# Optimization experiments

Measured on AMD Instinct MI355X. Metric: run time of the kernel, lower is better.

## Reference

```python
import jax, jax.numpy as jnp
import numpy as np
from functools import partial

K = 8  # seq_len from constructor


def _normalizer_impl(p, K):
    # 3-step Newton-Raphson solve for alpha s.t. sum_i (1 - exp(alpha*log(1-p_i))) == K
    N = p.shape[-1]
    y = jnp.log(1.0 - p)                        # (*, N)
    alpha = jnp.full(p.shape[:-1], float(K), dtype=p.dtype)
    for _ in range(3):
        e = jnp.exp(alpha[..., None] * y)       # (*, N)
        err = e.sum(axis=-1) + (K - N)          # (*,)
        d = (e * y).sum(axis=-1)                # (*,)
        alpha = alpha - err / d
    # analytic derivative used by the custom torch backward (ctx.deriv)
    deriv = alpha[..., None] * e / (d[..., None] * (1.0 - p))
    return alpha, deriv


@partial(jax.custom_vjp, nondiff_argnums=(1,))
def compute_normalizer(p, K):
    return _normalizer_impl(p, K)[0]


def _cn_fwd(p, K):
    alpha, deriv = _normalizer_impl(p, K)
    return alpha, deriv


def _cn_bwd(K, deriv, g):
    return (g[..., None] * deriv,)


compute_normalizer.defvjp(_cn_fwd, _cn_bwd)


def setup_inputs() -> dict:
    key = jax.random.key(0)
    k1, k2, k3 = jax.random.split(key, 3)
    B, T, F, N = 16, 2048, 512, 512
    x = jax.random.normal(k1, (B, T, F), dtype=jnp.float32)
    w_both = jax.random.normal(k2, (N, F), dtype=jnp.float32) * 0.05
    w_values = jax.random.normal(k3, (N, F), dtype=jnp.float32) * 0.05
    return {"x": x, "w_both": w_both, "w_values": w_values}


def reference(x, w_both, w_values):
    # probs = softmax(Linear(x)); values = softmax(probs + Linear(x))
    probs = jax.nn.softmax(jnp.einsum('btf,nf->btn', x, w_both), axis=-1)
    values = jax.nn.softmax(probs + jnp.einsum('btf,nf->btn', x, w_values), axis=-1)
    # marginals = 1 - (1 - probs) ** alpha, alpha from 3-step Newton normalizer
    alpha = compute_normalizer(probs, K)
    marginals = 1.0 - (1.0 - probs) ** alpha[..., None]
    # exclusive cumsum over classes
    cumsum = jnp.cumsum(probs, axis=-1) - probs
    return (marginals, values, cumsum)
```

## Files before the change

### kernel.cpp

```cpp
#include <hip/hip_runtime.h>
#include <hip/hip_bf16.h>
#include <stdint.h>

typedef __attribute__((ext_vector_type(8))) short bf16x8;
typedef __attribute__((ext_vector_type(4))) float f32x4;

typedef __attribute__((address_space(3))) char      lds_char;
typedef __attribute__((address_space(3))) unsigned  lds_uint;
typedef __attribute__((address_space(1))) const unsigned g_uint;

__device__ __forceinline__ unsigned short f2bf(float f) {
    unsigned u = __float_as_uint(f);
    unsigned r = (u + 0x7fffu + ((u >> 16) & 1u)) >> 16;
    return (unsigned short)r;
}

__device__ __forceinline__ void async_copy16(const void* g, lds_char* l) {
    __builtin_amdgcn_global_load_lds((g_uint*)g, (lds_uint*)l, 16, 0, 0);
}

__device__ __forceinline__ float wsum(float v) {
#pragma unroll
    for (int d = 32; d > 0; d >>= 1) v += __shfl_xor(v, d, 64);
    return v;
}
__device__ __forceinline__ float wmax(float v) {
#pragma unroll
    for (int d = 32; d > 0; d >>= 1) v = fmaxf(v, __shfl_xor(v, d, 64));
    return v;
}

#define BT_ROWS 32768
#define FDIM    512
#define NDIM    512
#define KSEQ    8.0f

__global__ __launch_bounds__(256) void cast_kernel(
    const float* __restrict__ x, const float* __restrict__ wb, const float* __restrict__ wv,
    unsigned short* __restrict__ xb, unsigned short* __restrict__ wbb, unsigned short* __restrict__ wvb)
{
    const int nx4 = (BT_ROWS * FDIM) >> 2;
    const int nw4 = (NDIM * FDIM) >> 2;
    int i = blockIdx.x * 256 + threadIdx.x;
    const float4* src; unsigned short* dst; int j;
    if (i < nx4)            { src = (const float4*)x;  dst = xb;  j = i; }
    else if (i < nx4 + nw4) { src = (const float4*)wb; dst = wbb; j = i - nx4; }
    else if (i < nx4+2*nw4) { src = (const float4*)wv; dst = wvb; j = i - nx4 - nw4; }
    else return;
    float4 v = src[j];
    ushort4 o;
    o.x = f2bf(v.x); o.y = f2bf(v.y); o.z = f2bf(v.z); o.w = f2bf(v.w);
    *(ushort4*)(dst + 4*(size_t)j) = o;
}

template<int BF16OUT>
__global__ __launch_bounds__(256) void gemm_kernel(
    const unsigned short* __restrict__ A,
    const unsigned short* __restrict__ W0,
    const unsigned short* __restrict__ W1,
    void* C0v, void* C1v)
{
    __shared__ unsigned short lds[8192];
    const int Kd = FDIM;
    const int t = threadIdx.x, w = t >> 6, l = t & 63;
    const int bn = blockIdx.x, bm = blockIdx.y, mat = blockIdx.z;
    const unsigned short* Wm = mat ? W1 : W0;
    void* Cv = mat ? C1v : C0v;

    const int srow  = (w << 4) + (l >> 2);
    const int skoff = (l & 3) << 3;
    const unsigned short* gA0 = A  + (size_t)(bm * 128 + srow) * Kd + skoff;
    const unsigned short* gA1 = gA0 + (size_t)64 * Kd;
    const unsigned short* gB0 = Wm + (size_t)(bn * 128 + srow) * Kd + skoff;
    const unsigned short* gB1 = gB0 + (size_t)64 * Kd;

    lds_char* lb = (lds_char*)lds;
    const unsigned offA0 = w * 1024;
    const unsigned offA1 = 4096 + w * 1024;
    const unsigned offB0 = 8192 + w * 1024;
    const unsigned offB1 = 12288 + w * 1024;

    const int wm = w >> 1, wn = w & 1;
    const int lr = l & 15, lk = (l >> 4) * 8;
    const unsigned short* lA = lds;
    const unsigned short* lB = lds + 4096;

    f32x4 acc[4][4] = {};

    const int ksteps = Kd / 32;
    for (int kk = 0; kk < ksteps; ++kk) {
        async_copy16(gA0, lb + offA0);
        async_copy16(gA1, lb + offA1);
        async_copy16(gB0, lb + offB0);
        async_copy16(gB1, lb + offB1);
        gA0 += 32; gA1 += 32; gB0 += 32; gB1 += 32;
        __syncthreads();

        bf16x8 ar[4], br[4];
#pragma unroll
        for (int r = 0; r < 4; ++r)
            ar[r] = *(const bf16x8*)&lA[(wm * 64 + r * 16 + lr) * 32 + lk];
#pragma unroll
        for (int c = 0; c < 4; ++c)
            br[c] = *(const bf16x8*)&lB[(wn * 64 + c * 16 + lr) * 32 + lk];
#pragma unroll
        for (int r = 0; r < 4; ++r)
#pragma unroll
            for (int c = 0; c < 4; ++c)
                acc[r][c] = __builtin_amdgcn_mfma_f32_16x16x32_bf16(ar[r], br[c], acc[r][c], 0, 0, 0);
        __syncthreads();
    }

    const int lg4 = (l >> 4) * 4;
#pragma unroll
    for (int r = 0; r < 4; ++r) {
        int row0 = bm * 128 + wm * 64 + r * 16 + lg4;
#pragma unroll
        for (int c = 0; c < 4; ++c) {
            int col = bn * 128 + wn * 64 + c * 16 + lr;
#pragma unroll
            for (int j = 0; j < 4; ++j) {
                if (BF16OUT) {
                    ((unsigned short*)Cv)[(size_t)(row0 + j) * NDIM + col] = f2bf(acc[r][c][j]);
                } else {
                    ((float*)Cv)[(size_t)(row0 + j) * NDIM + col] = acc[r][c][j];
                }
            }
        }
    }
}

template<int BF16IN>
__global__ __launch_bounds__(256) void rowwise_kernel(
    const void* Lbv, const void* Lvv, float* out)
{
    const size_t S = (size_t)BT_ROWS * NDIM;
    const int row = blockIdx.x * 4 + (threadIdx.x >> 6);
    const int l = threadIdx.x & 63;
    const size_t base = (size_t)row * NDIM + l * 8;

    float xb[8], xv[8];
    if (BF16IN) {
        uint4 ub = *(const uint4*)((const unsigned short*)Lbv + base);
        uint4 uv = *(const uint4*)((const unsigned short*)Lvv + base);
        unsigned b[4] = {ub.x, ub.y, ub.z, ub.w};
        unsigned v[4] = {uv.x, uv.y, uv.z, uv.w};
#pragma unroll
        for (int i = 0; i < 4; ++i) {
            xb[2*i]   = __uint_as_float(b[i] << 16);
            xb[2*i+1] = __uint_as_float(b[i] & 0xffff0000u);
            xv[2*i]   = __uint_as_float(v[i] << 16);
            xv[2*i+1] = __uint_as_float(v[i] & 0xffff0000u);
        }
    } else {
        const float4* fb = (const float4*)((const float*)Lbv + base);
        const float4* fv = (const float4*)((const float*)Lvv + base);
        float4 b0 = fb[0], b1 = fb[1], v0 = fv[0], v1 = fv[1];
        xb[0]=b0.x; xb[1]=b0.y; xb[2]=b0.z; xb[3]=b0.w;
        xb[4]=b1.x; xb[5]=b1.y; xb[6]=b1.z; xb[7]=b1.w;
        xv[0]=v0.x; xv[1]=v0.y; xv[2]=v0.z; xv[3]=v0.w;
        xv[4]=v1.x; xv[5]=v1.y; xv[6]=v1.z; xv[7]=v1.w;
    }

    float m1 = xb[0];
#pragma unroll
    for (int i = 1; i < 8; ++i) m1 = fmaxf(m1, xb[i]);
    m1 = wmax(m1);
    float p[8]; float s1 = 0.f;
#pragma unroll
    for (int i = 0; i < 8; ++i) { p[i] = __expf(xb[i] - m1); s1 += p[i]; }
    s1 = wsum(s1);
    float inv1 = 1.f / s1;
#pragma unroll
    for (int i = 0; i < 8; ++i) p[i] *= inv1;

    float tv[8];
    float m2 = -1e30f;
#pragma unroll
    for (int i = 0; i < 8; ++i) { tv[i] = p[i] + xv[i]; m2 = fmaxf(m2, tv[i]); }
    m2 = wmax(m2);
    float s2 = 0.f;
#pragma unroll
    for (int i = 0; i < 8; ++i) { tv[i] = __expf(tv[i] - m2); s2 += tv[i]; }
    s2 = wsum(s2);
    float inv2 = 1.f / s2;

    float y[8];
#pragma unroll
    for (int i = 0; i < 8; ++i) y[i] = __logf(1.0f - p[i]);
    float alpha = KSEQ;
#pragma unroll
    for (int it = 0; it < 3; ++it) {
        float se = 0.f, sd = 0.f;
#pragma unroll
        for (int i = 0; i < 8; ++i) {
            float e = __expf(alpha * y[i]);
            se += e; sd += e * y[i];
        }
        se = wsum(se); sd = wsum(sd);
        float err = se + (KSEQ - (float)NDIM);
        alpha = alpha - err / sd;
    }

    float mg[8];
#pragma unroll
    for (int i = 0; i < 8; ++i) mg[i] = 1.0f - __expf(alpha * y[i]);

    float loc = 0.f;
#pragma unroll
    for (int i = 0; i < 8; ++i) loc += p[i];
    float sc = loc;
#pragma unroll
    for (int d = 1; d < 64; d <<= 1) {
        float n = __shfl_up(sc, d, 64);
        if (l >= d) sc += n;
    }
    float run = sc - loc;
    float cum[8];
#pragma unroll
    for (int i = 0; i < 8; ++i) { cum[i] = run; run += p[i]; }

    float vals[8];
#pragma unroll
    for (int i = 0; i < 8; ++i) vals[i] = tv[i] * inv2;

    float4* omg = (float4*)(out + base);
    float4* ovl = (float4*)(out + S + base);
    float4* ocs = (float4*)(out + 2 * S + base);
    omg[0] = make_float4(mg[0], mg[1], mg[2], mg[3]);
    omg[1] = make_float4(mg[4], mg[5], mg[6], mg[7]);
    ovl[0] = make_float4(vals[0], vals[1], vals[2], vals[3]);
    ovl[1] = make_float4(vals[4], vals[5], vals[6], vals[7]);
    ocs[0] = make_float4(cum[0], cum[1], cum[2], cum[3]);
    ocs[1] = make_float4(cum[4], cum[5], cum[6], cum[7]);
}

extern "C" void kernel_launch(void* const* d_in, const int* in_sizes, int n_in,
                              void* d_out, int out_size, void* d_ws, size_t ws_size,
                              hipStream_t stream) {
    const float* x  = (const float*)d_in[0];
    const float* wb = (const float*)d_in[1];
    const float* wv = (const float*)d_in[2];
    float* out = (float*)d_out;
    char* ws = (char*)d_ws;
    const size_t S = (size_t)BT_ROWS * NDIM;

    unsigned short* xb  = (unsigned short*)(ws);
    unsigned short* wbb = (unsigned short*)(ws + 33554432);
    unsigned short* wvb = (unsigned short*)(ws + 34078720);
    unsigned short* lgb = (unsigned short*)(ws + 34603008);
    unsigned short* lgv = (unsigned short*)(ws + 68157440);
    const bool planA = ws_size >= (size_t)101711872;

    {
        int total4 = (BT_ROWS * FDIM + 2 * NDIM * FDIM) / 4;
        int blocks = (total4 + 255) / 256;
        cast_kernel<<<blocks, 256, 0, stream>>>(x, wb, wv, xb, wbb, wvb);
    }
    dim3 grid(NDIM / 128, BT_ROWS / 128, 2);
    if (planA) {
        gemm_kernel<1><<<grid, 256, 0, stream>>>(xb, wbb, wvb, (void*)lgb, (void*)lgv);
        rowwise_kernel<1><<<BT_ROWS / 4, 256, 0, stream>>>(lgb, lgv, out);
    } else {
        gemm_kernel<0><<<grid, 256, 0, stream>>>(xb, wbb, wvb, (void*)out, (void*)(out + S));
        rowwise_kernel<0><<<BT_ROWS / 4, 256, 0, stream>>>(out, out + S, out);
    }
}
```

Before: 328.3 us.

## Fuse x fp32-to-bf16 cast into GEMM and compute both projections per block

The separate cast of x to bf16 is dropped. The GEMM now loads fp32 x directly, packs it to bf16 in registers and stores it into a padded LDS tile, so one A tile feeds both weight matrices through a dual accumulator. The async global-to-LDS loads are replaced by register prefetch of the next k-step, which overlaps with the MFMA work, and a block-index swizzle is added for cache locality. This removes a 32MB write and read of bf16 x and halves the A-tile traffic, at the cost of more registers (two accumulator sets, occupancy hint of 2) and dropping the fp32 fallback path for small workspaces.

```diff
diff --git a/kernel.cpp b/kernel.cpp
--- a/kernel.cpp
+++ b/kernel.cpp
@@ -4,19 +4,14 @@
 
 typedef __attribute__((ext_vector_type(8))) short bf16x8;
 typedef __attribute__((ext_vector_type(4))) float f32x4;
-
-typedef __attribute__((address_space(3))) char      lds_char;
-typedef __attribute__((address_space(3))) unsigned  lds_uint;
-typedef __attribute__((address_space(1))) const unsigned g_uint;
 
 __device__ __forceinline__ unsigned short f2bf(float f) {
     unsigned u = __float_as_uint(f);
     unsigned r = (u + 0x7fffu + ((u >> 16) & 1u)) >> 16;
     return (unsigned short)r;
 }
-
-__device__ __forceinline__ void async_copy16(const void* g, lds_char* l) {
-    __builtin_amdgcn_global_load_lds((g_uint*)g, (lds_uint*)l, 16, 0, 0);
+__device__ __forceinline__ unsigned pack2(float lo, float hi) {
+    return (unsigned)f2bf(lo) | ((unsigned)f2bf(hi) << 16);
 }
 
 __device__ __forceinline__ float wsum(float v) {
@@ -34,81 +29,102 @@
 #define FDIM    512
 #define NDIM    512
 #define KSEQ    8.0f
-
-__global__ __launch_bounds__(256) void cast_kernel(
-    const float* __restrict__ x, const float* __restrict__ wb, const float* __restrict__ wv,
-    unsigned short* __restrict__ xb, unsigned short* __restrict__ wbb, unsigned short* __restrict__ wvb)
+#define LDW     40
+
+__global__ __launch_bounds__(256) void castw_kernel(
+    const float* __restrict__ wb, const float* __restrict__ wv,
+    unsigned short* __restrict__ wbb, unsigned short* __restrict__ wvb)
 {
-    const int nx4 = (BT_ROWS * FDIM) >> 2;
     const int nw4 = (NDIM * FDIM) >> 2;
     int i = blockIdx.x * 256 + threadIdx.x;
     const float4* src; unsigned short* dst; int j;
-    if (i < nx4)            { src = (const float4*)x;  dst = xb;  j = i; }
-    else if (i < nx4 + nw4) { src = (const float4*)wb; dst = wbb; j = i - nx4; }
-    else if (i < nx4+2*nw4) { src = (const float4*)wv; dst = wvb; j = i - nx4 - nw4; }
+    if (i < nw4)          { src = (const float4*)wb; dst = wbb; j = i; }
+    else if (i < 2 * nw4) { src = (const float4*)wv; dst = wvb; j = i - nw4; }
     else return;
     float4 v = src[j];
     ushort4 o;
     o.x = f2bf(v.x); o.y = f2bf(v.y); o.z = f2bf(v.z); o.w = f2bf(v.w);
-    *(ushort4*)(dst + 4*(size_t)j) = o;
-}
-
-template<int BF16OUT>
-__global__ __launch_bounds__(256) void gemm_kernel(
-    const unsigned short* __restrict__ A,
+    *(ushort4*)(dst + 4 * (size_t)j) = o;
+}
+
+__global__ __launch_bounds__(256, 2) void gemm2_kernel(
+    const float* __restrict__ X,
     const unsigned short* __restrict__ W0,
     const unsigned short* __restrict__ W1,
-    void* C0v, void* C1v)
+    unsigned short* __restrict__ C0,
+    unsigned short* __restrict__ C1)
 {
-    __shared__ unsigned short lds[8192];
-    const int Kd = FDIM;
+    __shared__ unsigned short lds[3 * 128 * LDW];
+    unsigned short* sA  = lds;
+    unsigned short* sB0 = lds + 128 * LDW;
+    unsigned short* sB1 = lds + 256 * LDW;
+
     const int t = threadIdx.x, w = t >> 6, l = t & 63;
-    const int bn = blockIdx.x, bm = blockIdx.y, mat = blockIdx.z;
-    const unsigned short* Wm = mat ? W1 : W0;
-    void* Cv = mat ? C1v : C0v;
-
-    const int srow  = (w << 4) + (l >> 2);
-    const int skoff = (l & 3) << 3;
-    const unsigned short* gA0 = A  + (size_t)(bm * 128 + srow) * Kd + skoff;
-    const unsigned short* gA1 = gA0 + (size_t)64 * Kd;
-    const unsigned short* gB0 = Wm + (size_t)(bn * 128 + srow) * Kd + skoff;
-    const unsigned short* gB1 = gB0 + (size_t)64 * Kd;
-
-    lds_char* lb = (lds_char*)lds;
-    const unsigned offA0 = w * 1024;
-    const unsigned offA1 = 4096 + w * 1024;
-    const unsigned offB0 = 8192 + w * 1024;
-    const unsigned offB1 = 12288 + w * 1024;
+
+    int swz = ((blockIdx.x & 7) << 7) + (blockIdx.x >> 3);
+    const int bm = swz >> 2, bn = swz & 3;
+
+    const int sr = t >> 1;
+    const int sk = (t & 1) << 4;
+    const float*          gX  = X  + (size_t)(bm * 128 + sr) * FDIM + sk;
+    const unsigned short* gB0 = W0 + (size_t)(bn * 128 + sr) * FDIM + sk;
+    const unsigned short* gB1 = W1 + (size_t)(bn * 128 + sr) * FDIM + sk;
+    const int wrow = sr * LDW + sk;
 
     const int wm = w >> 1, wn = w & 1;
     const int lr = l & 15, lk = (l >> 4) * 8;
-    const unsigned short* lA = lds;
-    const unsigned short* lB = lds + 4096;
-
-    f32x4 acc[4][4] = {};
-
-    const int ksteps = Kd / 32;
-    for (int kk = 0; kk < ksteps; ++kk) {
-        async_copy16(gA0, lb + offA0);
-        async_copy16(gA1, lb + offA1);
-        async_copy16(gB0, lb + offB0);
-        async_copy16(gB1, lb + offB1);
-        gA0 += 32; gA1 += 32; gB0 += 32; gB1 += 32;
+
+    f32x4 acc[2][4][4] = {};
+
+    float4 fa[4]; uint4 vb0[2], vb1[2];
+
+    auto LOADK = [&](int kk) {
+        const float* pa = gX + kk * 32;
+        fa[0] = *(const float4*)(pa);
+        fa[1] = *(const float4*)(pa + 4);
+        fa[2] = *(const float4*)(pa + 8);
+        fa[3] = *(const float4*)(pa + 12);
+        const uint4* p0 = (const uint4*)(gB0 + kk * 32);
+        vb0[0] = p0[0]; vb0[1] = p0[1];
+        const uint4* p1 = (const uint4*)(gB1 + kk * 32);
+        vb1[0] = p1[0]; vb1[1] = p1[1];
+    };
+
+    LOADK(0);
+    for (int kk = 0; kk < 16; ++kk) {
         __syncthreads();
-
-        bf16x8 ar[4], br[4];
+        {
+            uint4 a0, a1;
+            a0.x = pack2(fa[0].x, fa[0].y); a0.y = pack2(fa[0].z, fa[0].w);
+            a0.z = pack2(fa[1].x, fa[1].y); a0.w = pack2(fa[1].z, fa[1].w);
+            a1.x = pack2(fa[2].x, fa[2].y); a1.y = pack2(fa[2].z, fa[2].w);
+            a1.z = pack2(fa[3].x, fa[3].y); a1.w = pack2(fa[3].z, fa[3].w);
+            *(uint4*)&sA[wrow]      = a0;
+            *(uint4*)&sA[wrow + 8]  = a1;
+            *(uint4*)&sB0[wrow]     = vb0[0];
+            *(uint4*)&sB0[wrow + 8] = vb0[1];
+            *(uint4*)&sB1[wrow]     = vb1[0];
+            *(uint4*)&sB1[wrow + 8] = vb1[1];
+        }
+        __syncthreads();
+        if (kk < 15) LOADK(kk + 1);
+
+        bf16x8 ar[4], br0[4], br1[4];
 #pragma unroll
         for (int r = 0; r < 4; ++r)
-            ar[r] = *(const bf16x8*)&lA[(wm * 64 + r * 16 + lr) * 32 + lk];
-#pragma unroll
-        for (int c = 0; c < 4; ++c)
-            br[c] = *(const bf16x8*)&lB[(wn * 64 + c * 16 + lr) * 32 + lk];
+            ar[r] = *(const bf16x8*)&sA[(wm * 64 + r * 16 + lr) * LDW + lk];
+#pragma unroll
+        for (int c = 0; c < 4; ++c) {
+            br0[c] = *(const bf16x8*)&sB0[(wn * 64 + c * 16 + lr) * LDW + lk];
+            br1[c] = *(const bf16x8*)&sB1[(wn * 64 + c * 16 + lr) * LDW + lk];
+        }
 #pragma unroll
         for (int r = 0; r < 4; ++r)
 #pragma unroll
-            for (int c = 0; c < 4; ++c)
-                acc[r][c] = __builtin_amdgcn_mfma_f32_16x16x32_bf16(ar[r], br[c], acc[r][c], 0, 0, 0);
-        __syncthreads();
+            for (int c = 0; c < 4; ++c) {
+                acc[0][r][c] = __builtin_amdgcn_mfma_f32_16x16x32_bf16(ar[r], br0[c], acc[0][r][c], 0, 0, 0);
+                acc[1][r][c] = __builtin_amdgcn_mfma_f32_16x16x32_bf16(ar[r], br1[c], acc[1][r][c], 0, 0, 0);
+            }
     }
 
     const int lg4 = (l >> 4) * 4;
@@ -120,29 +136,27 @@
             int col = bn * 128 + wn * 64 + c * 16 + lr;
 #pragma unroll
             for (int j = 0; j < 4; ++j) {
-                if (BF16OUT) {
-                    ((unsigned short*)Cv)[(size_t)(row0 + j) * NDIM + col] = f2bf(acc[r][c][j]);
-                } else {
-                    ((float*)Cv)[(size_t)(row0 + j) * NDIM + col] = acc[r][c][j];
-                }
+                C0[(size_t)(row0 + j) * NDIM + col] = f2bf(acc[0][r][c][j]);
+                C1[(size_t)(row0 + j) * NDIM + col] = f2bf(acc[1][r][c][j]);
             }
         }
     }
 }
 
-template<int BF16IN>
 __global__ __launch_bounds__(256) void rowwise_kernel(
-    const void* Lbv, const void* Lvv, float* out)
+    const unsigned short* __restrict__ Lb,
+    const unsigned short* __restrict__ Lv,
+    float* __restrict__ out)
 {
     const size_t S = (size_t)BT_ROWS * NDIM;
     const int row = blockIdx.x * 4 + (threadIdx.x >> 6);
     const int l = threadIdx.x & 63;
     const size_t base = (size_t)row * NDIM + l * 8;
 
+    uint4 ub = *(const uint4*)(Lb + base);
+    uint4 uv = *(const uint4*)(Lv + base);
     float xb[8], xv[8];
-    if (BF16IN) {
-        uint4 ub = *(const uint4*)((const unsigned short*)Lbv + base);
-        uint4 uv = *(const uint4*)((const unsigned short*)Lvv + base);
+    {
         unsigned b[4] = {ub.x, ub.y, ub.z, ub.w};
         unsigned v[4] = {uv.x, uv.y, uv.z, uv.w};
 #pragma unroll
@@ -152,14 +166,6 @@
             xv[2*i]   = __uint_as_float(v[i] << 16);
             xv[2*i+1] = __uint_as_float(v[i] & 0xffff0000u);
         }
-    } else {
-        const float4* fb = (const float4*)((const float*)Lbv + base);
-        const float4* fv = (const float4*)((const float*)Lvv + base);
-        float4 b0 = fb[0], b1 = fb[1], v0 = fv[0], v1 = fv[1];
-        xb[0]=b0.x; xb[1]=b0.y; xb[2]=b0.z; xb[3]=b0.w;
-        xb[4]=b1.x; xb[5]=b1.y; xb[6]=b1.z; xb[7]=b1.w;
-        xv[0]=v0.x; xv[1]=v0.y; xv[2]=v0.z; xv[3]=v0.w;
-        xv[4]=v1.x; xv[5]=v1.y; xv[6]=v1.z; xv[7]=v1.w;
     }
 
     float m1 = xb[0];
@@ -243,26 +249,13 @@
     const float* wv = (const float*)d_in[2];
     float* out = (float*)d_out;
     char* ws = (char*)d_ws;
-    const size_t S = (size_t)BT_ROWS * NDIM;
-
-    unsigned short* xb  = (unsigned short*)(ws);
-    unsigned short* wbb = (unsigned short*)(ws + 33554432);
-    unsigned short* wvb = (unsigned short*)(ws + 34078720);
-    unsigned short* lgb = (unsigned short*)(ws + 34603008);
-    unsigned short* lgv = (unsigned short*)(ws + 68157440);
-    const bool planA = ws_size >= (size_t)101711872;
-
-    {
-        int total4 = (BT_ROWS * FDIM + 2 * NDIM * FDIM) / 4;
-        int blocks = (total4 + 255) / 256;
-        cast_kernel<<<blocks, 256, 0, stream>>>(x, wb, wv, xb, wbb, wvb);
-    }
-    dim3 grid(NDIM / 128, BT_ROWS / 128, 2);
-    if (planA) {
-        gemm_kernel<1><<<grid, 256, 0, stream>>>(xb, wbb, wvb, (void*)lgb, (void*)lgv);
-        rowwise_kernel<1><<<BT_ROWS / 4, 256, 0, stream>>>(lgb, lgv, out);
-    } else {
-        gemm_kernel<0><<<grid, 256, 0, stream>>>(xb, wbb, wvb, (void*)out, (void*)(out + S));
-        rowwise_kernel<0><<<BT_ROWS / 4, 256, 0, stream>>>(out, out + S, out);
-    }
-}
+
+    unsigned short* wbb = (unsigned short*)(ws);
+    unsigned short* wvb = (unsigned short*)(ws + 524288);
+    unsigned short* lgb = (unsigned short*)(ws + 1048576);
+    unsigned short* lgv = (unsigned short*)(ws + 1048576 + 33554432);
+
+    castw_kernel<<<512, 256, 0, stream>>>(wb, wv, wbb, wvb);
+    gemm2_kernel<<<1024, 256, 0, stream>>>(x, wbb, wvb, lgb, lgv);
+    rowwise_kernel<<<BT_ROWS / 4, 256, 0, stream>>>(lgb, lgv, out);
+}
```

Result: slower. 383.2 us (+16.7%).
